# Optimization experiments

Hardware: AMD Instinct MI355X
Metric: run time of the kernel (lower is better)

Reference implementation:

```python
import jax, jax.numpy as jnp
import numpy as np

N_POINTS = 131072
N_SEG = 16
C = 256
BN_EPS = 1e-5


def setup_inputs() -> dict:
    key = jax.random.key(0)
    ks = jax.random.split(key, 6)
    x = jax.random.normal(ks[0], (N_POINTS, C), jnp.float32)
    # Ragged segment end-offsets (cumulative counts), strictly increasing, last == N_POINTS.
    rng = np.random.default_rng(0)
    base = N_POINTS // N_SEG
    counts = base + rng.integers(-base // 32, base // 32, N_SEG)
    counts[-1] += N_POINTS - counts.sum()
    o = jnp.asarray(np.cumsum(counts), jnp.int32)
    s1 = 1.0 / np.sqrt(2 * C)  # linear1: Linear(2C -> C)
    s2 = 1.0 / np.sqrt(C)      # linear2: Linear(C -> C)
    W1 = jax.random.uniform(ks[1], (2 * C, C), jnp.float32, -s1, s1)
    b1 = jax.random.uniform(ks[2], (C,), jnp.float32, -s1, s1)
    W2 = jax.random.uniform(ks[3], (C, C), jnp.float32, -s2, s2)
    b2 = jax.random.uniform(ks[4], (C,), jnp.float32, -s2, s2)
    gamma = jnp.ones((C,), jnp.float32)
    beta = jnp.zeros((C,), jnp.float32)
    return {"x": x, "o": o, "W1": W1, "b1": b1, "W2": W2, "b2": b2,
            "gamma": gamma, "beta": beta}


def reference(x, o, W1, b1, W2, b2, gamma, beta):
    n, c = x.shape
    s = o.shape[0]
    # segment id per point from cumulative end-offsets
    seg_id = jnp.searchsorted(o, jnp.arange(n), side="right")  # [N]
    counts = jnp.concatenate([o[:1], o[1:] - o[:-1]])          # [S]
    # per-segment mean pooling (x_b.sum(0, True) / cnt)
    sums = jax.ops.segment_sum(x, seg_id, num_segments=s)      # [S, C]
    means = sums / counts[:, None].astype(x.dtype)
    # linear2: Linear(C, C) + ReLU on segment means
    y = jax.nn.relu(means @ W2 + b2)                           # [S, C]
    # broadcast-concat back to points, then linear1: Linear(2C, C)
    h = jnp.concatenate([x, y[seg_id]], axis=1) @ W1 + b1      # [N, C]
    # BatchNorm1d (training mode: batch statistics, biased variance) + ReLU
    mu = h.mean(axis=0)
    var = h.var(axis=0)
    out = jax.nn.relu((h - mu) * (gamma / jnp.sqrt(var + BN_EPS)) + beta)
    return out
```

## Files before the change

### kernel.cpp

```cpp
#include <hip/hip_runtime.h>
#include <hip/hip_bf16.h>
#include <stdint.h>

#define N_PTS 131072
#define NC 256
#define NSEG 16
#define BN_EPSF 1e-5f

typedef __attribute__((ext_vector_type(8))) short bf16x8;
typedef __attribute__((ext_vector_type(4))) float f32x4;

__device__ __forceinline__ unsigned short f2bf(float f) {
  union { float f; uint32_t u; } v; v.f = f;
  uint32_t u = v.u;
  uint32_t r = (u + 0x7fffu + ((u >> 16) & 1u)) >> 16;
  return (unsigned short)r;
}
__device__ __forceinline__ float bf2f(unsigned short h) {
  union { uint32_t u; float f; } v; v.u = ((uint32_t)h) << 16; return v.f;
}

__global__ void k_zero(float* __restrict__ p, int n) {
  int i = blockIdx.x * 256 + threadIdx.x;
  if (i < n) p[i] = 0.f;
}

__global__ __launch_bounds__(256) void k_segsum_convert(
    const float* __restrict__ x, const int* __restrict__ o,
    unsigned short* __restrict__ x_bf, float* __restrict__ seg_sums) {
  __shared__ int o_s[NSEG];
  __shared__ float s_acc[2][NC];
  int t = threadIdx.x;
  if (t < NSEG) o_s[t] = o[t];
  s_acc[0][t] = 0.f;
  s_acc[1][t] = 0.f;
  __syncthreads();
  int g = t >> 6, l = t & 63;
  int row0 = blockIdx.x * 64;
  int c0 = l * 4;
  int s0 = 0;
  while (o_s[s0] <= row0) ++s0;
  int e0 = o_s[s0];
  int s1 = (s0 < NSEG - 1) ? s0 + 1 : s0;
  float4 accA = {0.f, 0.f, 0.f, 0.f}, accB = {0.f, 0.f, 0.f, 0.f};
  const float4* xv = (const float4*)x;
#pragma unroll
  for (int i = 0; i < 16; ++i) {
    int r = row0 + g + i * 4;
    float4 v = xv[(size_t)r * 64 + l];
    ushort4 b;
    b.x = f2bf(v.x); b.y = f2bf(v.y); b.z = f2bf(v.z); b.w = f2bf(v.w);
    *(ushort4*)(x_bf + (size_t)r * NC + c0) = b;
    bool inA = (r < e0);
    accA.x += inA ? v.x : 0.f; accB.x += inA ? 0.f : v.x;
    accA.y += inA ? v.y : 0.f; accB.y += inA ? 0.f : v.y;
    accA.z += inA ? v.z : 0.f; accB.z += inA ? 0.f : v.z;
    accA.w += inA ? v.w : 0.f; accB.w += inA ? 0.f : v.w;
  }
  atomicAdd(&s_acc[0][c0 + 0], accA.x);
  atomicAdd(&s_acc[0][c0 + 1], accA.y);
  atomicAdd(&s_acc[0][c0 + 2], accA.z);
  atomicAdd(&s_acc[0][c0 + 3], accA.w);
  atomicAdd(&s_acc[1][c0 + 0], accB.x);
  atomicAdd(&s_acc[1][c0 + 1], accB.y);
  atomicAdd(&s_acc[1][c0 + 2], accB.z);
  atomicAdd(&s_acc[1][c0 + 3], accB.w);
  __syncthreads();
  atomicAdd(&seg_sums[s0 * NC + t], s_acc[0][t]);
  atomicAdd(&seg_sums[s1 * NC + t], s_acc[1][t]);
}

__global__ __launch_bounds__(256) void k_w1t(const float* __restrict__ W1,
                                             unsigned short* __restrict__ w1t) {
  __shared__ float tile[64][65];
  int t = threadIdx.x;
  int bx = blockIdx.x & 3, by = blockIdx.x >> 2;
  int k0 = by * 64, j0 = bx * 64;
  int r = t >> 6, c = t & 63;
#pragma unroll
  for (int i = 0; i < 16; ++i) {
    int kk = r + i * 4;
    tile[kk][c] = W1[(size_t)(k0 + kk) * NC + j0 + c];
  }
  __syncthreads();
#pragma unroll
  for (int i = 0; i < 16; ++i) {
    int jj = r + i * 4;
    w1t[(size_t)(j0 + jj) * NC + k0 + c] = f2bf(tile[c][jj]);
  }
}

__global__ __launch_bounds__(256) void k_seg_mlp(
    const int* __restrict__ o, const float* __restrict__ seg_sums,
    const float* __restrict__ W1, const float* __restrict__ b1,
    const float* __restrict__ W2, const float* __restrict__ b2,
    float* __restrict__ z) {
  __shared__ float mean_s[NC];
  __shared__ float y_s[NC];
  int b = blockIdx.x, j = threadIdx.x;
  int start = (b == 0) ? 0 : o[b - 1];
  float inv = 1.f / (float)(o[b] - start);
  mean_s[j] = seg_sums[b * NC + j] * inv;
  __syncthreads();
  float a = b2[j];
  for (int k = 0; k < NC; ++k) a += mean_s[k] * W2[k * NC + j];
  y_s[j] = fmaxf(a, 0.f);
  __syncthreads();
  float a2 = b1[j];
  for (int k = 0; k < NC; ++k) a2 += y_s[k] * W1[(NC + k) * NC + j];
  z[b * NC + j] = a2;
}

__global__ __launch_bounds__(256) void k_gemm(
    const unsigned short* __restrict__ x_bf, const unsigned short* __restrict__ w1t,
    const int* __restrict__ o, const float* __restrict__ z,
    unsigned short* __restrict__ h_bf,
    float* __restrict__ colsum, float* __restrict__ colsumsq) {
  __shared__ __align__(16) unsigned short lA[128 * 32];
  __shared__ __align__(16) unsigned short lB[128 * 32];
  __shared__ float s_sum[128];
  __shared__ float s_sq[128];
  __shared__ int o_s[NSEG];

  int t = threadIdx.x;
  int lane = t & 63, w = t >> 6;
  int wr = w >> 1, wc = w & 1;
  int bid = blockIdx.x;
  int ct = bid & 1, rt = bid >> 1;
  const int row0 = rt * 128, colT = ct * 128;

  if (t < 128) { s_sum[t] = 0.f; s_sq[t] = 0.f; }
  if (t < NSEG) o_s[t] = o[t];

  f32x4 acc[4][4] = {};

  for (int kt = 0; kt < 8; ++kt) {
    {
      int c = t;
      const unsigned short* ga = x_bf + (size_t)(row0 + (c >> 2)) * NC + kt * 32 + (c & 3) * 8;
      __builtin_amdgcn_global_load_lds(
          (const __attribute__((address_space(1))) void*)ga,
          (__attribute__((address_space(3))) void*)(lA + c * 8), 16, 0, 0);
      const unsigned short* gb = w1t + (size_t)(colT + (c >> 2)) * NC + kt * 32 + (c & 3) * 8;
      __builtin_amdgcn_global_load_lds(
          (const __attribute__((address_space(1))) void*)gb,
          (__attribute__((address_space(3))) void*)(lB + c * 8), 16, 0, 0);
      c = t + 256;
      ga = x_bf + (size_t)(row0 + (c >> 2)) * NC + kt * 32 + (c & 3) * 8;
      __builtin_amdgcn_global_load_lds(
          (const __attribute__((address_space(1))) void*)ga,
          (__attribute__((address_space(3))) void*)(lA + c * 8), 16, 0, 0);
      gb = w1t + (size_t)(colT + (c >> 2)) * NC + kt * 32 + (c & 3) * 8;
      __builtin_amdgcn_global_load_lds(
          (const __attribute__((address_space(1))) void*)gb,
          (__attribute__((address_space(3))) void*)(lB + c * 8), 16, 0, 0);
    }
    __syncthreads();
    bf16x8 af[4], bf[4];
#pragma unroll
    for (int m = 0; m < 4; ++m)
      af[m] = *(const bf16x8*)(lA + (wr * 64 + m * 16 + (lane & 15)) * 32 + (lane >> 4) * 8);
#pragma unroll
    for (int n = 0; n < 4; ++n)
      bf[n] = *(const bf16x8*)(lB + (wc * 64 + n * 16 + (lane & 15)) * 32 + (lane >> 4) * 8);
#pragma unroll
    for (int m = 0; m < 4; ++m)
#pragma unroll
      for (int n = 0; n < 4; ++n)
        acc[m][n] = __builtin_amdgcn_mfma_f32_16x16x32_bf16(af[m], bf[n], acc[m][n], 0, 0, 0);
    __syncthreads();
  }

  int s0 = 0;
  while (o_s[s0] <= row0) ++s0;
  int e0 = o_s[s0];
  int s1 = (s0 < NSEG - 1) ? s0 + 1 : s0;
  int cl = lane & 15, q = lane >> 4;
#pragma unroll
  for (int n = 0; n < 4; ++n) {
    int col = colT + wc * 64 + n * 16 + cl;
    float zA = z[s0 * NC + col], zB = z[s1 * NC + col];
    float ps = 0.f, pq = 0.f;
#pragma unroll
    for (int m = 0; m < 4; ++m) {
      int rbase = row0 + wr * 64 + m * 16 + q * 4;
#pragma unroll
      for (int r = 0; r < 4; ++r) {
        int row = rbase + r;
        float hv = acc[m][n][r] + ((row < e0) ? zA : zB);
        h_bf[(size_t)row * NC + col] = f2bf(hv);
        ps += hv; pq += hv * hv;
      }
    }
    ps += __shfl_xor(ps, 16, 64); ps += __shfl_xor(ps, 32, 64);
    pq += __shfl_xor(pq, 16, 64); pq += __shfl_xor(pq, 32, 64);
    if (q == 0) {
      atomicAdd(&s_sum[wc * 64 + n * 16 + cl], ps);
      atomicAdd(&s_sq[wc * 64 + n * 16 + cl], pq);
    }
  }
  __syncthreads();
  if (t < 128) {
    atomicAdd(&colsum[colT + t], s_sum[t]);
    atomicAdd(&colsumsq[colT + t], s_sq[t]);
  }
}

__global__ void k_bn_final(const float* __restrict__ colsum, const float* __restrict__ colsumsq,
                           const float* __restrict__ gamma, const float* __restrict__ beta,
                           float* __restrict__ scale, float* __restrict__ shift) {
  int t = threadIdx.x;
  float invN = 1.f / (float)N_PTS;
  float mu = colsum[t] * invN;
  float var = colsumsq[t] * invN - mu * mu;
  float sc = gamma[t] * rsqrtf(var + BN_EPSF);
  scale[t] = sc;
  shift[t] = beta[t] - mu * sc;
}

__global__ __launch_bounds__(256) void k_bn_apply(
    const unsigned short* __restrict__ h_bf, const float* __restrict__ scale,
    const float* __restrict__ shift, float* __restrict__ out) {
  int t = threadIdx.x;
  size_t idx = (size_t)blockIdx.x * 256 + t;
  size_t l0 = idx * 4;
  int col = (int)(l0 & 255);
  uint2 hv = *(const uint2*)(h_bf + l0);
  float4 sc = *(const float4*)(scale + col);
  float4 sh = *(const float4*)(shift + col);
  float f0 = bf2f((unsigned short)(hv.x & 0xffffu));
  float f1 = bf2f((unsigned short)(hv.x >> 16));
  float f2 = bf2f((unsigned short)(hv.y & 0xffffu));
  float f3 = bf2f((unsigned short)(hv.y >> 16));
  float4 o0;
  o0.x = fmaxf(f0 * sc.x + sh.x, 0.f);
  o0.y = fmaxf(f1 * sc.y + sh.y, 0.f);
  o0.z = fmaxf(f2 * sc.z + sh.z, 0.f);
  o0.w = fmaxf(f3 * sc.w + sh.w, 0.f);
  *(float4*)(out + l0) = o0;
}

extern "C" void kernel_launch(void* const* d_in, const int* in_sizes, int n_in,
                              void* d_out, int out_size, void* d_ws, size_t ws_size,
                              hipStream_t stream) {
  const float* x = (const float*)d_in[0];
  const int* o = (const int*)d_in[1];
  const float* W1 = (const float*)d_in[2];
  const float* b1 = (const float*)d_in[3];
  const float* W2 = (const float*)d_in[4];
  const float* b2 = (const float*)d_in[5];
  const float* gamma = (const float*)d_in[6];
  const float* beta = (const float*)d_in[7];
  float* out = (float*)d_out;

  char* ws = (char*)d_ws;
  unsigned short* x_bf = (unsigned short*)ws;
  unsigned short* h_bf = (unsigned short*)(ws + 67108864);
  char* base2 = ws + 134217728;
  float* seg_sums = (float*)(base2);
  float* colsum   = (float*)(base2 + 16384);
  float* colsumsq = (float*)(base2 + 17408);
  float* z        = (float*)(base2 + 18432);
  float* scale    = (float*)(base2 + 34816);
  float* shift    = (float*)(base2 + 35840);
  unsigned short* w1t = (unsigned short*)(base2 + 36864);

  k_zero<<<18, 256, 0, stream>>>(seg_sums, 4608);
  k_segsum_convert<<<2048, 256, 0, stream>>>(x, o, x_bf, seg_sums);
  k_w1t<<<16, 256, 0, stream>>>(W1, w1t);
  k_seg_mlp<<<16, 256, 0, stream>>>(o, seg_sums, W1, b1, W2, b2, z);
  k_gemm<<<2048, 256, 0, stream>>>(x_bf, w1t, o, z, h_bf, colsum, colsumsq);
  k_bn_final<<<1, 256, 0, stream>>>(colsum, colsumsq, gamma, beta, scale, shift);
  k_bn_apply<<<32768, 256, 0, stream>>>(h_bf, scale, shift, out);
}
```

Measured before the change: 349.6 us.

## Recompute GEMM for output instead of storing bf16 h; fuse BN apply into GEMM

Drops the bf16 intermediate h buffer. A first GEMM pass only accumulates the column sum and sum of squares, and a second GEMM pass recomputes h and applies BN scale/shift and ReLU directly in the epilogue. Tiles become 64 rows by all 256 columns with K-steps of 64, and an XOR swizzle is applied to x_bf and w1t so LDS reads avoid bank conflicts. The zeroing and W1 transpose kernels are merged into one prep launch. The cost is doubled GEMM compute and a second read of x_bf, traded against the h write and read traffic and the separate BN kernels.

```diff
diff --git a/kernel.cpp b/kernel.cpp
--- a/kernel.cpp
+++ b/kernel.cpp
@@ -1,5 +1,4 @@
 #include <hip/hip_runtime.h>
-#include <hip/hip_bf16.h>
 #include <stdint.h>
 
 #define N_PTS 131072
@@ -16,13 +15,42 @@
   uint32_t r = (u + 0x7fffu + ((u >> 16) & 1u)) >> 16;
   return (unsigned short)r;
 }
-__device__ __forceinline__ float bf2f(unsigned short h) {
-  union { uint32_t u; float f; } v; v.u = ((uint32_t)h) << 16; return v.f;
-}
-
-__global__ void k_zero(float* __restrict__ p, int n) {
-  int i = blockIdx.x * 256 + threadIdx.x;
-  if (i < n) p[i] = 0.f;
+
+__device__ __forceinline__ int swz(int col, int row) {
+  return (col & ~63) | ((((col >> 3) & 7) ^ (row & 7)) << 3) | (col & 7);
+}
+
+__device__ __forceinline__ void gll16(const unsigned short* g, unsigned short* l) {
+  __builtin_amdgcn_global_load_lds(
+      (const __attribute__((address_space(1))) void*)g,
+      (__attribute__((address_space(3))) void*)l, 16, 0, 0);
+}
+
+__global__ __launch_bounds__(256) void k_prep(const float* __restrict__ W1,
+                                              unsigned short* __restrict__ w1t,
+                                              float* __restrict__ zerobuf) {
+  int b = blockIdx.x, t = threadIdx.x;
+  if (b >= 16) {
+    int i = (b - 16) * 256 + t;
+    if (i < 4608) zerobuf[i] = 0.f;
+    return;
+  }
+  __shared__ float tile[64][65];
+  int bx = b & 3, by = b >> 2;
+  int k0 = by * 64, j0 = bx * 64;
+  int r = t >> 6, c = t & 63;
+#pragma unroll
+  for (int i = 0; i < 16; ++i) {
+    int kk = r + i * 4;
+    tile[kk][c] = W1[(size_t)(k0 + kk) * NC + j0 + c];
+  }
+  __syncthreads();
+#pragma unroll
+  for (int i = 0; i < 16; ++i) {
+    int jj = r + i * 4;
+    int row = j0 + jj, col = k0 + c;
+    w1t[(size_t)row * NC + swz(col, row)] = f2bf(tile[c][jj]);
+  }
 }
 
 __global__ __launch_bounds__(256) void k_segsum_convert(
@@ -50,7 +78,7 @@
     float4 v = xv[(size_t)r * 64 + l];
     ushort4 b;
     b.x = f2bf(v.x); b.y = f2bf(v.y); b.z = f2bf(v.z); b.w = f2bf(v.w);
-    *(ushort4*)(x_bf + (size_t)r * NC + c0) = b;
+    *(ushort4*)(x_bf + (size_t)r * NC + swz(c0, r)) = b;
     bool inA = (r < e0);
     accA.x += inA ? v.x : 0.f; accB.x += inA ? 0.f : v.x;
     accA.y += inA ? v.y : 0.f; accB.y += inA ? 0.f : v.y;
@@ -68,26 +96,6 @@
   __syncthreads();
   atomicAdd(&seg_sums[s0 * NC + t], s_acc[0][t]);
   atomicAdd(&seg_sums[s1 * NC + t], s_acc[1][t]);
-}
-
-__global__ __launch_bounds__(256) void k_w1t(const float* __restrict__ W1,
-                                             unsigned short* __restrict__ w1t) {
-  __shared__ float tile[64][65];
-  int t = threadIdx.x;
-  int bx = blockIdx.x & 3, by = blockIdx.x >> 2;
-  int k0 = by * 64, j0 = bx * 64;
-  int r = t >> 6, c = t & 63;
-#pragma unroll
-  for (int i = 0; i < 16; ++i) {
-    int kk = r + i * 4;
-    tile[kk][c] = W1[(size_t)(k0 + kk) * NC + j0 + c];
-  }
-  __syncthreads();
-#pragma unroll
-  for (int i = 0; i < 16; ++i) {
-    int jj = r + i * 4;
-    w1t[(size_t)(j0 + jj) * NC + k0 + c] = f2bf(tile[c][jj]);
-  }
 }
 
 __global__ __launch_bounds__(256) void k_seg_mlp(
@@ -111,63 +119,50 @@
   z[b * NC + j] = a2;
 }
 
-__global__ __launch_bounds__(256) void k_gemm(
+__global__ __launch_bounds__(256) void k_gemm_stats(
     const unsigned short* __restrict__ x_bf, const unsigned short* __restrict__ w1t,
     const int* __restrict__ o, const float* __restrict__ z,
-    unsigned short* __restrict__ h_bf,
     float* __restrict__ colsum, float* __restrict__ colsumsq) {
-  __shared__ __align__(16) unsigned short lA[128 * 32];
-  __shared__ __align__(16) unsigned short lB[128 * 32];
-  __shared__ float s_sum[128];
-  __shared__ float s_sq[128];
+  __shared__ __align__(16) unsigned short lA[64 * 64];
+  __shared__ __align__(16) unsigned short lB[256 * 64];
+  __shared__ float s_sum[NC], s_sq[NC];
   __shared__ int o_s[NSEG];
-
-  int t = threadIdx.x;
-  int lane = t & 63, w = t >> 6;
-  int wr = w >> 1, wc = w & 1;
-  int bid = blockIdx.x;
-  int ct = bid & 1, rt = bid >> 1;
-  const int row0 = rt * 128, colT = ct * 128;
-
-  if (t < 128) { s_sum[t] = 0.f; s_sq[t] = 0.f; }
+  int t = threadIdx.x, lane = t & 63, w = t >> 6;
+  int row0 = blockIdx.x * 64;
   if (t < NSEG) o_s[t] = o[t];
 
   f32x4 acc[4][4] = {};
-
-  for (int kt = 0; kt < 8; ++kt) {
-    {
-      int c = t;
-      const unsigned short* ga = x_bf + (size_t)(row0 + (c >> 2)) * NC + kt * 32 + (c & 3) * 8;
-      __builtin_amdgcn_global_load_lds(
-          (const __attribute__((address_space(1))) void*)ga,
-          (__attribute__((address_space(3))) void*)(lA + c * 8), 16, 0, 0);
-      const unsigned short* gb = w1t + (size_t)(colT + (c >> 2)) * NC + kt * 32 + (c & 3) * 8;
-      __builtin_amdgcn_global_load_lds(
-          (const __attribute__((address_space(1))) void*)gb,
-          (__attribute__((address_space(3))) void*)(lB + c * 8), 16, 0, 0);
-      c = t + 256;
-      ga = x_bf + (size_t)(row0 + (c >> 2)) * NC + kt * 32 + (c & 3) * 8;
-      __builtin_amdgcn_global_load_lds(
-          (const __attribute__((address_space(1))) void*)ga,
-          (__attribute__((address_space(3))) void*)(lA + c * 8), 16, 0, 0);
-      gb = w1t + (size_t)(colT + (c >> 2)) * NC + kt * 32 + (c & 3) * 8;
-      __builtin_amdgcn_global_load_lds(
-          (const __attribute__((address_space(1))) void*)gb,
-          (__attribute__((address_space(3))) void*)(lB + c * 8), 16, 0, 0);
+  for (int kt = 0; kt < 4; ++kt) {
+    gll16(x_bf + (size_t)(row0 + (t >> 3)) * NC + kt * 64 + (t & 7) * 8, lA + t * 8);
+    gll16(x_bf + (size_t)(row0 + (t >> 3) + 32) * NC + kt * 64 + (t & 7) * 8,
+          lA + (t + 256) * 8);
+#pragma unroll
+    for (int i = 0; i < 8; ++i) {
+      int tp = t + i * 256;
+      gll16(w1t + (size_t)(tp >> 3) * NC + kt * 64 + (t & 7) * 8, lB + tp * 8);
     }
     __syncthreads();
-    bf16x8 af[4], bf[4];
-#pragma unroll
-    for (int m = 0; m < 4; ++m)
-      af[m] = *(const bf16x8*)(lA + (wr * 64 + m * 16 + (lane & 15)) * 32 + (lane >> 4) * 8);
-#pragma unroll
-    for (int n = 0; n < 4; ++n)
-      bf[n] = *(const bf16x8*)(lB + (wc * 64 + n * 16 + (lane & 15)) * 32 + (lane >> 4) * 8);
-#pragma unroll
-    for (int m = 0; m < 4; ++m)
-#pragma unroll
-      for (int n = 0; n < 4; ++n)
-        acc[m][n] = __builtin_amdgcn_mfma_f32_16x16x32_bf16(af[m], bf[n], acc[m][n], 0, 0, 0);
+#pragma unroll
+    for (int kk = 0; kk < 2; ++kk) {
+      bf16x8 af[4], bfr[4];
+      int sl = kk * 4 + (lane >> 4);
+#pragma unroll
+      for (int mm = 0; mm < 4; ++mm) {
+        int r = mm * 16 + (lane & 15);
+        af[mm] = *(const bf16x8*)(lA + r * 64 + ((sl ^ (r & 7)) << 3));
+      }
+#pragma unroll
+      for (int nn = 0; nn < 4; ++nn) {
+        int jrow = w * 64 + nn * 16 + (lane & 15);
+        bfr[nn] = *(const bf16x8*)(lB + jrow * 64 + ((sl ^ (jrow & 7)) << 3));
+      }
+#pragma unroll
+      for (int mm = 0; mm < 4; ++mm)
+#pragma unroll
+        for (int nn = 0; nn < 4; ++nn)
+          acc[mm][nn] = __builtin_amdgcn_mfma_f32_16x16x32_bf16(af[mm], bfr[nn],
+                                                                acc[mm][nn], 0, 0, 0);
+    }
     __syncthreads();
   }
 
@@ -177,67 +172,108 @@
   int s1 = (s0 < NSEG - 1) ? s0 + 1 : s0;
   int cl = lane & 15, q = lane >> 4;
 #pragma unroll
-  for (int n = 0; n < 4; ++n) {
-    int col = colT + wc * 64 + n * 16 + cl;
+  for (int nn = 0; nn < 4; ++nn) {
+    int col = w * 64 + nn * 16 + cl;
     float zA = z[s0 * NC + col], zB = z[s1 * NC + col];
     float ps = 0.f, pq = 0.f;
 #pragma unroll
-    for (int m = 0; m < 4; ++m) {
-      int rbase = row0 + wr * 64 + m * 16 + q * 4;
+    for (int mm = 0; mm < 4; ++mm) {
 #pragma unroll
       for (int r = 0; r < 4; ++r) {
-        int row = rbase + r;
-        float hv = acc[m][n][r] + ((row < e0) ? zA : zB);
-        h_bf[(size_t)row * NC + col] = f2bf(hv);
+        int row = row0 + mm * 16 + q * 4 + r;
+        float hv = acc[mm][nn][r] + ((row < e0) ? zA : zB);
         ps += hv; pq += hv * hv;
       }
     }
     ps += __shfl_xor(ps, 16, 64); ps += __shfl_xor(ps, 32, 64);
     pq += __shfl_xor(pq, 16, 64); pq += __shfl_xor(pq, 32, 64);
-    if (q == 0) {
-      atomicAdd(&s_sum[wc * 64 + n * 16 + cl], ps);
-      atomicAdd(&s_sq[wc * 64 + n * 16 + cl], pq);
-    }
-  }
-  __syncthreads();
-  if (t < 128) {
-    atomicAdd(&colsum[colT + t], s_sum[t]);
-    atomicAdd(&colsumsq[colT + t], s_sq[t]);
-  }
-}
-
-__global__ void k_bn_final(const float* __restrict__ colsum, const float* __restrict__ colsumsq,
-                           const float* __restrict__ gamma, const float* __restrict__ beta,
-                           float* __restrict__ scale, float* __restrict__ shift) {
-  int t = threadIdx.x;
-  float invN = 1.f / (float)N_PTS;
-  float mu = colsum[t] * invN;
-  float var = colsumsq[t] * invN - mu * mu;
-  float sc = gamma[t] * rsqrtf(var + BN_EPSF);
-  scale[t] = sc;
-  shift[t] = beta[t] - mu * sc;
-}
-
-__global__ __launch_bounds__(256) void k_bn_apply(
-    const unsigned short* __restrict__ h_bf, const float* __restrict__ scale,
-    const float* __restrict__ shift, float* __restrict__ out) {
-  int t = threadIdx.x;
-  size_t idx = (size_t)blockIdx.x * 256 + t;
-  size_t l0 = idx * 4;
-  int col = (int)(l0 & 255);
-  uint2 hv = *(const uint2*)(h_bf + l0);
-  float4 sc = *(const float4*)(scale + col);
-  float4 sh = *(const float4*)(shift + col);
-  float f0 = bf2f((unsigned short)(hv.x & 0xffffu));
-  float f1 = bf2f((unsigned short)(hv.x >> 16));
-  float f2 = bf2f((unsigned short)(hv.y & 0xffffu));
-  float f3 = bf2f((unsigned short)(hv.y >> 16));
-  float4 o0;
-  o0.x = fmaxf(f0 * sc.x + sh.x, 0.f);
-  o0.y = fmaxf(f1 * sc.y + sh.y, 0.f);
-  o0.z = fmaxf(f2 * sc.z + sh.z, 0.f);
-  o0.w = fmaxf(f3 * sc.w + sh.w, 0.f);
-  *(float4*)(out + l0) = o0;
+    if (q == 0) { s_sum[col] = ps; s_sq[col] = pq; }
+  }
+  __syncthreads();
+  atomicAdd(&colsum[t], s_sum[t]);
+  atomicAdd(&colsumsq[t], s_sq[t]);
+}
+
+__global__ __launch_bounds__(256) void k_gemm_out(
+    const unsigned short* __restrict__ x_bf, const unsigned short* __restrict__ w1t,
+    const int* __restrict__ o, const float* __restrict__ z,
+    const float* __restrict__ colsum, const float* __restrict__ colsumsq,
+    const float* __restrict__ gamma, const float* __restrict__ beta,
+    float* __restrict__ out) {
+  __shared__ __align__(16) unsigned short lA[64 * 64];
+  __shared__ __align__(16) unsigned short lB[256 * 64];
+  __shared__ float s_scale[NC], s_shift[NC];
+  __shared__ int o_s[NSEG];
+  int t = threadIdx.x, lane = t & 63, w = t >> 6;
+  int row0 = blockIdx.x * 64;
+  {
+    float invN = 1.f / (float)N_PTS;
+    float mu = colsum[t] * invN;
+    float var = colsumsq[t] * invN - mu * mu;
+    float sc = gamma[t] * rsqrtf(var + BN_EPSF);
+    s_scale[t] = sc;
+    s_shift[t] = beta[t] - mu * sc;
+  }
+  if (t < NSEG) o_s[t] = o[t];
+
+  f32x4 acc[4][4] = {};
+  for (int kt = 0; kt < 4; ++kt) {
+    gll16(x_bf + (size_t)(row0 + (t >> 3)) * NC + kt * 64 + (t & 7) * 8, lA + t * 8);
+    gll16(x_bf + (size_t)(row0 + (t >> 3) + 32) * NC + kt * 64 + (t & 7) * 8,
+          lA + (t + 256) * 8);
+#pragma unroll
+    for (int i = 0; i < 8; ++i) {
+      int tp = t + i * 256;
+      gll16(w1t + (size_t)(tp >> 3) * NC + kt * 64 + (t & 7) * 8, lB + tp * 8);
+    }
+    __syncthreads();
+#pragma unroll
+    for (int kk = 0; kk < 2; ++kk) {
+      bf16x8 af[4], bfr[4];
+      int sl = kk * 4 + (lane >> 4);
+#pragma unroll
+      for (int mm = 0; mm < 4; ++mm) {
+        int r = mm * 16 + (lane & 15);
+        af[mm] = *(const bf16x8*)(lA + r * 64 + ((sl ^ (r & 7)) << 3));
+      }
+#pragma unroll
+      for (int nn = 0; nn < 4; ++nn) {
+        int jrow = w * 64 + nn * 16 + (lane & 15);
+        bfr[nn] = *(const bf16x8*)(lB + jrow * 64 + ((sl ^ (jrow & 7)) << 3));
+      }
+#pragma unroll
+      for (int mm = 0; mm < 4; ++mm)
+#pragma unroll
+        for (int nn = 0; nn < 4; ++nn)
+          acc[mm][nn] = __builtin_amdgcn_mfma_f32_16x16x32_bf16(bfr[nn], af[mm],
+                                                                acc[mm][nn], 0, 0, 0);
+    }
+    __syncthreads();
+  }
+
+  int s0 = 0;
+  while (o_s[s0] <= row0) ++s0;
+  int e0 = o_s[s0];
+  int s1 = (s0 < NSEG - 1) ? s0 + 1 : s0;
+  int rl = lane & 15, q = lane >> 4;
+#pragma unroll
+  for (int mm = 0; mm < 4; ++mm) {
+    int row = row0 + mm * 16 + rl;
+    int sg = (row < e0) ? s0 : s1;
+#pragma unroll
+    for (int nn = 0; nn < 4; ++nn) {
+      int c = w * 64 + nn * 16 + q * 4;
+      float4 z4 = *(const float4*)(z + sg * NC + c);
+      float4 sc4 = *(const float4*)(s_scale + c);
+      float4 sh4 = *(const float4*)(s_shift + c);
+      float4 o4;
+      o4.x = fmaxf((acc[mm][nn][0] + z4.x) * sc4.x + sh4.x, 0.f);
+      o4.y = fmaxf((acc[mm][nn][1] + z4.y) * sc4.y + sh4.y, 0.f);
+      o4.z = fmaxf((acc[mm][nn][2] + z4.z) * sc4.z + sh4.z, 0.f);
+      o4.w = fmaxf((acc[mm][nn][3] + z4.w) * sc4.w + sh4.w, 0.f);
+      *(float4*)(out + (size_t)row * NC + c) = o4;
+    }
+  }
 }
 
 extern "C" void kernel_launch(void* const* d_in, const int* in_sizes, int n_in,
@@ -255,21 +291,17 @@
 
   char* ws = (char*)d_ws;
   unsigned short* x_bf = (unsigned short*)ws;
-  unsigned short* h_bf = (unsigned short*)(ws + 67108864);
-  char* base2 = ws + 134217728;
+  char* base2 = ws + 67108864;
   float* seg_sums = (float*)(base2);
   float* colsum   = (float*)(base2 + 16384);
   float* colsumsq = (float*)(base2 + 17408);
   float* z        = (float*)(base2 + 18432);
-  float* scale    = (float*)(base2 + 34816);
-  float* shift    = (float*)(base2 + 35840);
-  unsigned short* w1t = (unsigned short*)(base2 + 36864);
-
-  k_zero<<<18, 256, 0, stream>>>(seg_sums, 4608);
+  unsigned short* w1t = (unsigned short*)(base2 + 34816);
+
+  k_prep<<<34, 256, 0, stream>>>(W1, w1t, seg_sums);
   k_segsum_convert<<<2048, 256, 0, stream>>>(x, o, x_bf, seg_sums);
-  k_w1t<<<16, 256, 0, stream>>>(W1, w1t);
   k_seg_mlp<<<16, 256, 0, stream>>>(o, seg_sums, W1, b1, W2, b2, z);
-  k_gemm<<<2048, 256, 0, stream>>>(x_bf, w1t, o, z, h_bf, colsum, colsumsq);
-  k_bn_final<<<1, 256, 0, stream>>>(colsum, colsumsq, gamma, beta, scale, shift);
-  k_bn_apply<<<32768, 256, 0, stream>>>(h_bf, scale, shift, out);
-}
+  k_gemm_stats<<<2048, 256, 0, stream>>>(x_bf, w1t, o, z, colsum, colsumsq);
+  k_gemm_out<<<2048, 256, 0, stream>>>(x_bf, w1t, o, z, colsum, colsumsq,
+                                       gamma, beta, out);
+}
```

Result: slower. 364.9 us (+4.4%).
